# Kernel optimization log

Measured on AMD Instinct MI355X. Metric: run time of the kernel, lower is better.

Reference implementation:

```python
import jax, jax.numpy as jnp
import numpy as np

NEG_MIN = float(np.finfo(np.float32).min)
LN_EPS = 1e-05


def _layer_norm(x, g, b):
    m = jnp.mean(x, axis=-1, keepdims=True)
    v = jnp.var(x, axis=-1, keepdims=True)
    return (x - m) * jax.lax.rsqrt(v + LN_EPS) * g + b


def _rel_shift_uni(x):
    # x: [qlen, rlen, bsz, n_head] -- Transformer-XL relative shift
    q, r, b, n = x.shape
    zero_pad = jnp.zeros((q, 1, b, n), x.dtype)
    x_padded = jnp.concatenate([zero_pad, x], axis=1).reshape(r + 1, q, b, n)
    return x_padded[1:].reshape(q, r, b, n)


def setup_inputs() -> dict:
    key = jax.random.key(0)
    ks = jax.random.split(key, 12)
    qlen, bsz, d_model = 2048, 2, 1024
    n_head, d_head, d_inner = 16, 64, 4096

    w = jax.random.normal(ks[0], (qlen, bsz, d_model), dtype=jnp.float32)

    # sinusoidal relative position embedding, positions klen-1 .. 0
    pos_seq = jnp.arange(qlen - 1, -1, -1, dtype=jnp.float32)
    inv_freq = 1.0 / (10000.0 ** (jnp.arange(0, d_model, 2, dtype=jnp.float32) / d_model))
    sinusoid = pos_seq[:, None] * inv_freq[None, :]
    r = jnp.concatenate([jnp.sin(sinusoid), jnp.cos(sinusoid)], axis=-1)  # [qlen, d_model]

    s = 0.02
    r_w_bias = jax.random.normal(ks[1], (n_head, d_head), dtype=jnp.float32) * s
    r_r_bias = jax.random.normal(ks[2], (n_head, d_head), dtype=jnp.float32) * s
    qkv_w = jax.random.normal(ks[3], (d_model, 3 * n_head * d_head), dtype=jnp.float32) * s
    r_net_w = jax.random.normal(ks[4], (d_model, n_head * d_head), dtype=jnp.float32) * s
    o_w = jax.random.normal(ks[5], (n_head * d_head, d_model), dtype=jnp.float32) * s
    ffn_w1 = jax.random.normal(ks[6], (d_model, d_inner), dtype=jnp.float32) * s
    ffn_b1 = jnp.zeros((d_inner,), dtype=jnp.float32)
    ffn_w2 = jax.random.normal(ks[7], (d_inner, d_model), dtype=jnp.float32) * s
    ffn_b2 = jnp.zeros((d_model,), dtype=jnp.float32)
    ln1_g = jnp.ones((d_model,), dtype=jnp.float32)
    ln1_b = jnp.zeros((d_model,), dtype=jnp.float32)
    ln2_g = jnp.ones((d_model,), dtype=jnp.float32)
    ln2_b = jnp.zeros((d_model,), dtype=jnp.float32)

    # causal mask: position j > i is masked (uni-directional attention)
    attn_mask = jnp.triu(jnp.ones((qlen, qlen), dtype=bool), k=1)

    return {"w": w, "r": r, "r_w_bias": r_w_bias, "r_r_bias": r_r_bias,
            "attn_mask": attn_mask, "qkv_w": qkv_w, "r_net_w": r_net_w, "o_w": o_w,
            "ln1_g": ln1_g, "ln1_b": ln1_b, "ffn_w1": ffn_w1, "ffn_b1": ffn_b1,
            "ffn_w2": ffn_w2, "ffn_b2": ffn_b2, "ln2_g": ln2_g, "ln2_b": ln2_b}


def reference(w, r, r_w_bias, r_r_bias, attn_mask, qkv_w, r_net_w, o_w,
              ln1_g, ln1_b, ffn_w1, ffn_b1, ffn_w2, ffn_b2, ln2_g, ln2_b):
    qlen, bsz, d_model = w.shape
    n_head, d_head = r_w_bias.shape
    scale = 1.0 / (d_head ** 0.5)

    # qkv projection (post-lnorm path: no pre-norm)
    w_heads = w @ qkv_w  # [q, b, 3*n*d]
    w_q, w_k, w_v = jnp.split(w_heads, 3, axis=-1)
    w_q = w_q.reshape(qlen, bsz, n_head, d_head)
    w_k = w_k.reshape(qlen, bsz, n_head, d_head)
    w_v = w_v.reshape(qlen, bsz, n_head, d_head)

    r_k = (r @ r_net_w).reshape(r.shape[0], n_head, d_head)  # [rlen, n, d]

    # AC: content term, BD: position term with rel-shift
    AC = jnp.einsum('ibnd,jbnd->ijbn', w_q + r_w_bias, w_k)
    BD = jnp.einsum('ibnd,jnd->ijbn', w_q + r_r_bias, r_k)
    BD = _rel_shift_uni(BD)

    attn_score = (AC + BD) * scale
    attn_score = jnp.where(attn_mask[:, :, None, None], NEG_MIN, attn_score)
    attn_prob = jax.nn.softmax(attn_score, axis=1)  # softmax over key axis j

    attn_vec = jnp.einsum('ijbn,jbnd->ibnd', attn_prob, w_v)
    attn_vec = attn_vec.reshape(qlen, bsz, n_head * d_head)
    attn_out = attn_vec @ o_w

    x = _layer_norm(w + attn_out, ln1_g, ln1_b)  # post-lnorm

    # PositionwiseFF (post-lnorm, eval: dropout inactive)
    core = jax.nn.relu(x @ ffn_w1 + ffn_b1) @ ffn_w2 + ffn_b2
    out = _layer_norm(x + core, ln2_g, ln2_b)
    return out
```

## Files before the change

### kernel.cpp

```cpp
#include <hip/hip_runtime.h>
#include <math.h>


typedef __attribute__((ext_vector_type(8))) short short8;
typedef __attribute__((ext_vector_type(4))) float floatx4;

__device__ inline unsigned short f2bf(float f) {
  union { float f; unsigned u; } v; v.f = f;
  unsigned r = v.u + 0x7FFFu + ((v.u >> 16) & 1u);
  return (unsigned short)(r >> 16);
}
__device__ inline float bf2f(unsigned short u) {
  union { unsigned u; float f; } v; v.u = ((unsigned)u) << 16; return v.f;
}

__global__ __launch_bounds__(256) void prep_kernel(
    const float* __restrict__ w, unsigned short* __restrict__ wb,
    const float* __restrict__ r, unsigned short* __restrict__ rb,
    const float* __restrict__ qkv_w, unsigned short* __restrict__ qkvT,
    const float* __restrict__ r_net_w, unsigned short* __restrict__ rnetT,
    const float* __restrict__ o_w, unsigned short* __restrict__ owT,
    const float* __restrict__ ffn_w1, unsigned short* __restrict__ w1T,
    const float* __restrict__ ffn_w2, unsigned short* __restrict__ w2T) {
  __shared__ __align__(16) unsigned short Ts[64][68];
  const int blk = blockIdx.x;
  const int t = threadIdx.x;
  if (blk < 6144) {
    const float* in = blk < 4096 ? w : r;
    unsigned short* outp = blk < 4096 ? wb : rb;
    const int i = (blk < 4096 ? blk : blk - 4096) * 256 + t;
    float4 v = ((const float4*)in)[i];
    ((ushort4*)outp)[i] =
        make_ushort4(f2bf(v.x), f2bf(v.y), f2bf(v.z), f2bf(v.w));
    return;
  }
  const float* src; unsigned short* dst; int K, N, idx;
  if (blk < 6912)      { src = qkv_w;   dst = qkvT;  K = 1024; N = 3072; idx = blk - 6144; }
  else if (blk < 7168) { src = r_net_w; dst = rnetT; K = 1024; N = 1024; idx = blk - 6912; }
  else if (blk < 7424) { src = o_w;     dst = owT;   K = 1024; N = 1024; idx = blk - 7168; }
  else if (blk < 8448) { src = ffn_w1;  dst = w1T;   K = 1024; N = 4096; idx = blk - 7424; }
  else                 { src = ffn_w2;  dst = w2T;   K = 4096; N = 1024; idx = blk - 8448; }
  const int nbx = N >> 6;
  const int k0 = (idx / nbx) * 64, n0 = (idx % nbx) * 64;
  const int rr = t >> 4, c = (t & 15) * 4;
#pragma unroll
  for (int rb2 = 0; rb2 < 64; rb2 += 16) {
    float4 v = *(const float4*)(src + (size_t)(k0 + rb2 + rr) * N + n0 + c);
    *(ushort4*)&Ts[rb2 + rr][c] =
        make_ushort4(f2bf(v.x), f2bf(v.y), f2bf(v.z), f2bf(v.w));
  }
  __syncthreads();
#pragma unroll
  for (int rb2 = 0; rb2 < 64; rb2 += 16) {
    const int nn = rb2 + rr;
    ushort4 o = make_ushort4(Ts[c + 0][nn], Ts[c + 1][nn],
                             Ts[c + 2][nn], Ts[c + 3][nn]);
    *(ushort4*)(dst + (size_t)(n0 + nn) * K + k0 + c) = o;
  }
}

template<int BIAS, int RELU, int OUT_BF16>
__device__ __forceinline__ void bgemm_body(
    const unsigned short* __restrict__ A, const unsigned short* __restrict__ Bt,
    const float* __restrict__ bias, void* __restrict__ C,
    int M, int N, int Kstride, int Klen, size_t psize,
    int bx, int by, int kz,
    unsigned short* As, unsigned short* Bs) {
  const int t = threadIdx.x;
  const int wv = t >> 6, lane = t & 63, quad = lane >> 4, lq = lane & 15;
  const int m0 = by * 128, n0 = bx * 128;
  const int wvm = (wv >> 1) * 64, wvn = (wv & 1) * 64;

  const int srow = t >> 2;
  const int scol = (t & 3) * 8;
  const size_t koff = (size_t)kz * Klen;
  const unsigned short* Ag = A + (size_t)(m0 + srow) * Kstride + scol + koff;
  const unsigned short* Bg = Bt + (size_t)(n0 + srow) * Kstride + scol + koff;
  unsigned short* AsW0 = As + (size_t)wv * 512;
  unsigned short* AsW1 = As + 4096 + (size_t)wv * 512;
  unsigned short* BsW0 = Bs + (size_t)wv * 512;
  unsigned short* BsW1 = Bs + 4096 + (size_t)wv * 512;

  floatx4 acc[4][4];
#pragma unroll
  for (int am = 0; am < 4; ++am)
#pragma unroll
    for (int bn = 0; bn < 4; ++bn) acc[am][bn] = (floatx4){0.f, 0.f, 0.f, 0.f};

  for (int k0 = 0; k0 < Klen; k0 += 64) {
    __syncthreads();
    __builtin_amdgcn_global_load_lds(
        (const __attribute__((address_space(1))) void*)(Ag + k0),
        (__attribute__((address_space(3))) void*)AsW0, 16, 0, 0);
    __builtin_amdgcn_global_load_lds(
        (const __attribute__((address_space(1))) void*)(Ag + (size_t)64 * Kstride + k0),
        (__attribute__((address_space(3))) void*)(AsW0 + 64 * 32), 16, 0, 0);
    __builtin_amdgcn_global_load_lds(
        (const __attribute__((address_space(1))) void*)(Ag + k0 + 32),
        (__attribute__((address_space(3))) void*)AsW1, 16, 0, 0);
    __builtin_amdgcn_global_load_lds(
        (const __attribute__((address_space(1))) void*)(Ag + (size_t)64 * Kstride + k0 + 32),
        (__attribute__((address_space(3))) void*)(AsW1 + 64 * 32), 16, 0, 0);
    __builtin_amdgcn_global_load_lds(
        (const __attribute__((address_space(1))) void*)(Bg + k0),
        (__attribute__((address_space(3))) void*)BsW0, 16, 0, 0);
    __builtin_amdgcn_global_load_lds(
        (const __attribute__((address_space(1))) void*)(Bg + (size_t)64 * Kstride + k0),
        (__attribute__((address_space(3))) void*)(BsW0 + 64 * 32), 16, 0, 0);
    __builtin_amdgcn_global_load_lds(
        (const __attribute__((address_space(1))) void*)(Bg + k0 + 32),
        (__attribute__((address_space(3))) void*)BsW1, 16, 0, 0);
    __builtin_amdgcn_global_load_lds(
        (const __attribute__((address_space(1))) void*)(Bg + (size_t)64 * Kstride + k0 + 32),
        (__attribute__((address_space(3))) void*)(BsW1 + 64 * 32), 16, 0, 0);
    __syncthreads();

#pragma unroll
    for (int s = 0; s < 2; ++s) {
      const unsigned short* Asub = s ? As + 4096 : As;
      const unsigned short* Bsub = s ? Bs + 4096 : Bs;
      short8 af[4], bf[4];
#pragma unroll
      for (int am = 0; am < 4; ++am)
        af[am] = *(const short8*)&Asub[(wvm + am * 16 + lq) * 32 + quad * 8];
#pragma unroll
      for (int bn = 0; bn < 4; ++bn)
        bf[bn] = *(const short8*)&Bsub[(wvn + bn * 16 + lq) * 32 + quad * 8];
#pragma unroll
      for (int am = 0; am < 4; ++am)
#pragma unroll
        for (int bn = 0; bn < 4; ++bn)
          acc[am][bn] = __builtin_amdgcn_mfma_f32_16x16x32_bf16(
              af[am], bf[bn], acc[am][bn], 0, 0, 0);
    }
  }

  float bs[4] = {0.f, 0.f, 0.f, 0.f};
  if (BIAS) {
    if (kz == 0) {
#pragma unroll
      for (int bn = 0; bn < 4; ++bn) bs[bn] = bias[n0 + wvn + bn * 16 + lq];
    }
  }
  float* Cf = (float*)C + (size_t)kz * psize;
#pragma unroll
  for (int am = 0; am < 4; ++am) {
#pragma unroll
    for (int u = 0; u < 4; ++u) {
      const size_t row = m0 + wvm + am * 16 + quad * 4 + u;
#pragma unroll
      for (int bn = 0; bn < 4; ++bn) {
        const size_t col = n0 + wvn + bn * 16 + lq;
        float v = acc[am][bn][u];
        if (BIAS) v += bs[bn];
        if (RELU) v = fmaxf(v, 0.f);
        if (OUT_BF16) ((unsigned short*)C)[row * N + col] = f2bf(v);
        else          Cf[row * N + col] = v;
      }
    }
  }
}

template<int BIAS, int RELU, int OUT_BF16>
__global__ __launch_bounds__(256) void bgemm_kernel(
    const unsigned short* __restrict__ A, const unsigned short* __restrict__ Bt,
    const float* __restrict__ bias, void* __restrict__ C,
    int M, int N, int Kstride, int Klen, size_t psize) {
  __shared__ __align__(16) unsigned short As[2 * 128 * 32];
  __shared__ __align__(16) unsigned short Bs[2 * 128 * 32];
  bgemm_body<BIAS, RELU, OUT_BF16>(A, Bt, bias, C, M, N, Kstride, Klen, psize,
                                   blockIdx.x, blockIdx.y, blockIdx.z, As, Bs);
}

__global__ __launch_bounds__(256) void qkv_rk_kernel(
    const unsigned short* __restrict__ wb, const unsigned short* __restrict__ qkvT,
    unsigned short* __restrict__ w_heads,
    const unsigned short* __restrict__ rbf, const unsigned short* __restrict__ rnetT,
    unsigned short* __restrict__ rk) {
  __shared__ __align__(16) unsigned short As[2 * 128 * 32];
  __shared__ __align__(16) unsigned short Bs[2 * 128 * 32];
  const int bid = blockIdx.x;
  if (bid < 768) {
    bgemm_body<0, 0, 1>(wb, qkvT, nullptr, w_heads, 4096, 3072, 1024, 1024, 0,
                        bid % 24, bid / 24, 0, As, Bs);
  } else {
    const int b2 = bid - 768;
    bgemm_body<0, 0, 1>(rbf, rnetT, nullptr, rk, 2048, 1024, 1024, 1024, 0,
                        b2 % 8, b2 / 8, 0, As, Bs);
  }
}

__global__ __launch_bounds__(512, 4) void attn_mfma_kernel(
    const unsigned short* __restrict__ w_heads,
    const unsigned short* __restrict__ r_k,
    const float* __restrict__ r_w_bias, const float* __restrict__ r_r_bias,
    unsigned short* __restrict__ attn_vec) {
  __shared__ __align__(16) unsigned short Ks[64 * 72];
  __shared__ __align__(16) unsigned short Vt[64 * 72];
  __shared__ __align__(16) unsigned short Rb[256 * 72];
  __shared__ __align__(16) unsigned short Pl[8 * 16 * 72];

  const int t = threadIdx.x;
  const int wv = t >> 6, lane = t & 63, quad = lane >> 4, lq = lane & 15;
  const int g = blockIdx.x;
  const int qq = g >> 5, bnb = g & 31;
  const int it = (qq < 8) ? (15 - qq) : (qq - 8);
  const int b = bnb & 1, n = bnb >> 1;
  const int i0 = it * 128, iw = i0 + wv * 16;

  const int kr = t >> 3, kc8 = (t & 7) * 8;
  const int vj = t & 31, vc = (t >> 5) * 4;

  short8 qw[2], qr[2];
  {
    const unsigned short* qrow =
        w_heads + (size_t)((iw + lq) * 2 + b) * 3072 + n * 64;
    short8 a0 = *(const short8*)(qrow + quad * 8);
    short8 a1 = *(const short8*)(qrow + 32 + quad * 8);
    const float* wbp = r_w_bias + n * 64;
    const float* rbp = r_r_bias + n * 64;
#pragma unroll
    for (int j = 0; j < 8; ++j) {
      const int k0 = quad * 8 + j, k1 = 32 + quad * 8 + j;
      const float q0 = bf2f((unsigned short)a0[j]);
      const float q1 = bf2f((unsigned short)a1[j]);
      qw[0][j] = (short)f2bf(q0 + wbp[k0]);
      qr[0][j] = (short)f2bf(q0 + rbp[k0]);
      qw[1][j] = (short)f2bf(q1 + wbp[k1]);
      qr[1][j] = (short)f2bf(q1 + rbp[k1]);
    }
  }

  floatx4 o[4];
#pragma unroll
  for (int dt = 0; dt < 4; ++dt) o[dt] = (floatx4){0.f, 0.f, 0.f, 0.f};
  float lrow[4] = {0.f, 0.f, 0.f, 0.f};

  unsigned short* Pw = Pl + wv * (16 * 72);
  const int wb2 = 112 - wv * 16;

  int g_idx[4]; bool g_hi[4];
#pragma unroll
  for (int u = 0; u < 4; ++u) {
    const int s = 15 - (quad * 4 + u);
    g_idx[u] = quad * 16 + ((s + lq) & 15);
    g_hi[u] = (s + lq) >= 16;
  }

  const int pbase0 = 1920 - i0;
  const int jt_end = 2 * it + 2;

#pragma unroll
  for (int bq = 0; bq < 2; ++bq) {
    const int row = pbase0 + bq * 64 + kr;
    const int slot = row & 255;
    *(short8*)&Rb[slot * 72 + kc8] =
        *(const short8*)(r_k + (size_t)row * 1024 + n * 64 + kc8);
  }
  short8 sK, sR;
  ushort4 sVl, sVh;
  {
    const unsigned short* kb =
        w_heads + (size_t)(kr * 2 + b) * 3072 + n * 64 + 1024 + kc8;
    sK = *(const short8*)kb;
    const unsigned short* vbp =
        w_heads + (size_t)((2 * vj) * 2 + b) * 3072 + n * 64 + 2048 + vc;
    sVl = *(const ushort4*)vbp;
    sVh = *(const ushort4*)(vbp + 2 * 3072);
    int pg = pbase0 + 128 + kr; if (pg > 2047) pg = 2047;
    sR = *(const short8*)(r_k + (size_t)pg * 1024 + n * 64 + kc8);
  }

  for (int jt = 0; jt < jt_end; ++jt) {
    const int j0 = jt * 64;
    const int pbase = pbase0 + 64 * jt;

    asm volatile("" ::: "memory");
    __builtin_amdgcn_s_barrier();
    asm volatile("" ::: "memory");

    *(short8*)&Ks[kr * 72 + kc8] = sK;
#pragma unroll
    for (int i2 = 0; i2 < 4; ++i2)
      *(unsigned*)&Vt[(vc + i2) * 72 + 2 * vj] =
          (unsigned)sVl[i2] | ((unsigned)sVh[i2] << 16);
    {
      const int slot = (pbase + 128 + kr) & 255;
      *(short8*)&Rb[slot * 72 + kc8] = sR;
    }

    if (jt + 1 < jt_end) {
      const int j0n = j0 + 64;
      const unsigned short* kb =
          w_heads + (size_t)((j0n + kr) * 2 + b) * 3072 + n * 64 + 1024 + kc8;
      sK = *(const short8*)kb;
      const unsigned short* vbp =
          w_heads + (size_t)((j0n + 2 * vj) * 2 + b) * 3072 + n * 64 + 2048 + vc;
      sVl = *(const ushort4*)vbp;
      sVh = *(const ushort4*)(vbp + 2 * 3072);
      int pg = pbase + 192 + kr; if (pg > 2047) pg = 2047;
      sR = *(const short8*)(r_k + (size_t)pg * 1024 + n * 64 + kc8);
    }

    asm volatile("s_waitcnt lgkmcnt(0)" ::: "memory");
    __builtin_amdgcn_s_barrier();
    asm volatile("" ::: "memory");

    floatx4 ac[4];
#pragma unroll
    for (int ct = 0; ct < 4; ++ct) {
      short8 b0 = *(const short8*)&Ks[(ct * 16 + lq) * 72 + quad * 8];
      short8 b1 = *(const short8*)&Ks[(ct * 16 + lq) * 72 + 32 + quad * 8];
      floatx4 z = (floatx4){0.f, 0.f, 0.f, 0.f};
      z = __builtin_amdgcn_mfma_f32_16x16x32_bf16(qw[0], b0, z, 0, 0, 0);
      z = __builtin_amdgcn_mfma_f32_16x16x32_bf16(qw[1], b1, z, 0, 0, 0);
      ac[ct] = z;
    }
    floatx4 Tt[5];
#pragma unroll
    for (int pt = 0; pt < 5; ++pt) {
      const int slot = (pbase + wb2 + pt * 16 + lq) & 255;
      short8 b0 = *(const short8*)&Rb[slot * 72 + quad * 8];
      short8 b1 = *(const short8*)&Rb[slot * 72 + 32 + quad * 8];
      floatx4 z = (floatx4){0.f, 0.f, 0.f, 0.f};
      z = __builtin_amdgcn_mfma_f32_16x16x32_bf16(qr[0], b0, z, 0, 0, 0);
      z = __builtin_amdgcn_mfma_f32_16x16x32_bf16(qr[1], b1, z, 0, 0, 0);
      Tt[pt] = z;
    }

    const bool interior = (j0 + 63 <= iw);
    if (interior) {
#pragma unroll
      for (int u = 0; u < 4; ++u) {
        const int r = quad * 4 + u;
        float sh[5];
#pragma unroll
        for (int pt = 0; pt < 5; ++pt) sh[pt] = __shfl(Tt[pt][u], g_idx[u]);
#pragma unroll
        for (int ct = 0; ct < 4; ++ct) {
          const float bd = g_hi[u] ? sh[ct + 1] : sh[ct];
          const float xs = (ac[ct][u] + bd) * 0.18033688011112042f;
          float pr; asm("v_exp_f32 %0, %1" : "=v"(pr) : "v"(xs));
          Pw[r * 72 + ct * 16 + lq] = f2bf(pr);
          lrow[u] += pr;
        }
      }
    } else {
#pragma unroll
      for (int u = 0; u < 4; ++u) {
        const int r = quad * 4 + u, i = iw + r;
        float sh[5];
#pragma unroll
        for (int pt = 0; pt < 5; ++pt) sh[pt] = __shfl(Tt[pt][u], g_idx[u]);
#pragma unroll
        for (int ct = 0; ct < 4; ++ct) {
          const float bd = g_hi[u] ? sh[ct + 1] : sh[ct];
          const int j = j0 + ct * 16 + lq;
          const float xs = (ac[ct][u] + bd) * 0.18033688011112042f;
          float pr; asm("v_exp_f32 %0, %1" : "=v"(pr) : "v"(xs));
          pr = (j <= i) ? pr : 0.f;
          Pw[r * 72 + ct * 16 + lq] = f2bf(pr);
          lrow[u] += pr;
        }
      }
    }

    __builtin_amdgcn_s_waitcnt(0xC07F);

    short8 pA0 = *(const short8*)&Pw[lq * 72 + quad * 8];
    short8 pA1 = *(const short8*)&Pw[lq * 72 + 32 + quad * 8];
#pragma unroll
    for (int dt = 0; dt < 4; ++dt) {
      short8 v0 = *(const short8*)&Vt[(dt * 16 + lq) * 72 + quad * 8];
      short8 v1 = *(const short8*)&Vt[(dt * 16 + lq) * 72 + 32 + quad * 8];
      o[dt] = __builtin_amdgcn_mfma_f32_16x16x32_bf16(pA0, v0, o[dt], 0, 0, 0);
      o[dt] = __builtin_amdgcn_mfma_f32_16x16x32_bf16(pA1, v1, o[dt], 0, 0, 0);
    }
  }

#pragma unroll
  for (int u = 0; u < 4; ++u) {
    float l = lrow[u];
    l += __shfl_xor(l, 1);
    l += __shfl_xor(l, 2);
    l += __shfl_xor(l, 4);
    l += __shfl_xor(l, 8);
    const float linv = 1.f / l;
    const int i = iw + quad * 4 + u;
    unsigned short* op = attn_vec + (size_t)(i * 2 + b) * 1024 + n * 64 + lq;
#pragma unroll
    for (int dt = 0; dt < 4; ++dt) op[dt * 16] = f2bf(o[dt][u] * linv);
  }
}

__global__ __launch_bounds__(256) void ln_res_kernel(
    const float* __restrict__ X, const float* __restrict__ R0,
    const float* __restrict__ R1,
    const float* __restrict__ g, const float* __restrict__ bta,
    float* __restrict__ out, unsigned short* __restrict__ out_bf) {
  const int row = blockIdx.x;
  const int t = threadIdx.x;
  float4 xv = ((const float4*)(X + (size_t)row * 1024))[t];
  float4 rv = ((const float4*)(R0 + (size_t)row * 1024))[t];
  float4 v = make_float4(xv.x + rv.x, xv.y + rv.y, xv.z + rv.z, xv.w + rv.w);
  if (R1) {
    float4 r2 = ((const float4*)(R1 + (size_t)row * 1024))[t];
    v.x += r2.x; v.y += r2.y; v.z += r2.z; v.w += r2.w;
  }
  float s  = v.x + v.y + v.z + v.w;
  float sq = v.x * v.x + v.y * v.y + v.z * v.z + v.w * v.w;
#pragma unroll
  for (int off = 32; off > 0; off >>= 1) {
    s  += __shfl_xor(s, off);
    sq += __shfl_xor(sq, off);
  }
  __shared__ float ss[4], ssq[4];
  const int wid = t >> 6;
  if ((t & 63) == 0) { ss[wid] = s; ssq[wid] = sq; }
  __syncthreads();
  s  = ss[0] + ss[1] + ss[2] + ss[3];
  sq = ssq[0] + ssq[1] + ssq[2] + ssq[3];
  const float mean = s * (1.f / 1024.f);
  const float var  = sq * (1.f / 1024.f) - mean * mean;
  const float inv  = rsqrtf(var + 1e-5f);
  float4 gv = ((const float4*)g)[t];
  float4 bv = ((const float4*)bta)[t];
  float4 ov = make_float4((v.x - mean) * inv * gv.x + bv.x,
                          (v.y - mean) * inv * gv.y + bv.y,
                          (v.z - mean) * inv * gv.z + bv.z,
                          (v.w - mean) * inv * gv.w + bv.w);
  ((float4*)(out + (size_t)row * 1024))[t] = ov;
  if (out_bf)
    ((ushort4*)(out_bf + (size_t)row * 1024))[t] =
        make_ushort4(f2bf(ov.x), f2bf(ov.y), f2bf(ov.z), f2bf(ov.w));
}

extern "C" void kernel_launch(void* const* d_in, const int* in_sizes, int n_in,
                              void* d_out, int out_size, void* d_ws, size_t ws_size,
                              hipStream_t stream) {
  (void)in_sizes; (void)n_in; (void)out_size; (void)ws_size;
  const float* w        = (const float*)d_in[0];
  const float* r        = (const float*)d_in[1];
  const float* r_w_bias = (const float*)d_in[2];
  const float* r_r_bias = (const float*)d_in[3];
  const float* qkv_w    = (const float*)d_in[5];
  const float* r_net_w  = (const float*)d_in[6];
  const float* o_w      = (const float*)d_in[7];
  const float* ln1_g    = (const float*)d_in[8];
  const float* ln1_b    = (const float*)d_in[9];
  const float* ffn_w1   = (const float*)d_in[10];
  const float* ffn_b1   = (const float*)d_in[11];
  const float* ffn_w2   = (const float*)d_in[12];
  const float* ffn_b2   = (const float*)d_in[13];
  const float* ln2_g    = (const float*)d_in[14];
  const float* ln2_b    = (const float*)d_in[15];
  float* out = (float*)d_out;

  char* base = (char*)d_ws;
  const size_t MB = (size_t)1 << 20;
  unsigned short* w_heads = (unsigned short*)(base + 0);
  float*          aout0   = (float*)(base + 0);
  float*          aout1   = (float*)(base + 16 * MB);
  unsigned short* h1      = (unsigned short*)(base + 0);
  float*          x       = (float*)(base + 32 * MB);
  unsigned short* w2T     = (unsigned short*)(base + 48 * MB);
  unsigned short* w1T     = (unsigned short*)(base + 56 * MB);
  float*          core0   = (float*)(base + 56 * MB);
  float*          core1   = (float*)(base + 72 * MB);
  unsigned short* wb      = (unsigned short*)(base + 64 * MB);
  unsigned short* avec    = (unsigned short*)(base + 64 * MB);
  unsigned short* rb      = (unsigned short*)(base + 72 * MB);
  unsigned short* xb      = (unsigned short*)(base + 72 * MB);
  unsigned short* rk      = (unsigned short*)(base + 76 * MB);
  unsigned short* qkvT    = (unsigned short*)(base + 80 * MB);
  unsigned short* owT     = (unsigned short*)(base + 86 * MB);
  unsigned short* rnetT   = (unsigned short*)(base + 88 * MB);

  dim3 blk(256);
  prep_kernel<<<9472, blk, 0, stream>>>(w, wb, r, rb, qkv_w, qkvT,
                                        r_net_w, rnetT, o_w, owT,
                                        ffn_w1, w1T, ffn_w2, w2T);

  qkv_rk_kernel<<<896, blk, 0, stream>>>(wb, qkvT, w_heads, rb, rnetT, rk);
  attn_mfma_kernel<<<512, 512, 0, stream>>>(
      w_heads, rk, r_w_bias, r_r_bias, avec);
  bgemm_kernel<0, 0, 0><<<dim3(8, 32, 2), blk, 0, stream>>>(
      avec, owT, nullptr, aout0, 4096, 1024, 1024, 512, (size_t)4096 * 1024);
  ln_res_kernel<<<4096, blk, 0, stream>>>(w, aout0, aout1, ln1_g, ln1_b, x, xb);
  bgemm_kernel<1, 1, 1><<<dim3(32, 32, 1), blk, 0, stream>>>(
      xb, w1T, ffn_b1, h1, 4096, 4096, 1024, 1024, 0);
  bgemm_kernel<1, 0, 0><<<dim3(8, 32, 2), blk, 0, stream>>>(
      h1, w2T, ffn_b2, core0, 4096, 1024, 4096, 2048, (size_t)4096 * 1024);
  ln_res_kernel<<<4096, blk, 0, stream>>>(x, core0, core1, ln2_g, ln2_b, out, nullptr);
}
```

Before: 418.2 us.

## Add 256x256 double-buffered GEMM for QKV/r_k and FFN1 projections

Introduces a new GEMM body with 256x256 output tiles, 512 threads, K-step 64 and double-buffered LDS staging, so the next tile's global-to-LDS loads overlap MFMA compute. It replaces the 128x128 single-buffer GEMM for the fused QKV/r_k launch and the FFN first layer. Larger tiles cut global/L2 traffic per FLOP but use 128KB of LDS per block and many accumulator registers, which lowers occupancy and leaves fewer blocks (224 and 256) to fill the CUs. The LDS layout with 64-element rows and no padding may cause bank conflicts.

```diff
diff --git a/kernel.cpp b/kernel.cpp
--- a/kernel.cpp
+++ b/kernel.cpp
@@ -13,6 +13,11 @@
 __device__ inline float bf2f(unsigned short u) {
   union { unsigned u; float f; } v; v.u = ((unsigned)u) << 16; return v.f;
 }
+
+#define G2L(gp, lp)                                                  \
+  __builtin_amdgcn_global_load_lds(                                  \
+      (const __attribute__((address_space(1))) void*)(gp),           \
+      (__attribute__((address_space(3))) void*)(lp), 16, 0, 0)
 
 __global__ __launch_bounds__(256) void prep_kernel(
     const float* __restrict__ w, unsigned short* __restrict__ wb,
@@ -89,30 +94,14 @@
 
   for (int k0 = 0; k0 < Klen; k0 += 64) {
     __syncthreads();
-    __builtin_amdgcn_global_load_lds(
-        (const __attribute__((address_space(1))) void*)(Ag + k0),
-        (__attribute__((address_space(3))) void*)AsW0, 16, 0, 0);
-    __builtin_amdgcn_global_load_lds(
-        (const __attribute__((address_space(1))) void*)(Ag + (size_t)64 * Kstride + k0),
-        (__attribute__((address_space(3))) void*)(AsW0 + 64 * 32), 16, 0, 0);
-    __builtin_amdgcn_global_load_lds(
-        (const __attribute__((address_space(1))) void*)(Ag + k0 + 32),
-        (__attribute__((address_space(3))) void*)AsW1, 16, 0, 0);
-    __builtin_amdgcn_global_load_lds(
-        (const __attribute__((address_space(1))) void*)(Ag + (size_t)64 * Kstride + k0 + 32),
-        (__attribute__((address_space(3))) void*)(AsW1 + 64 * 32), 16, 0, 0);
-    __builtin_amdgcn_global_load_lds(
-        (const __attribute__((address_space(1))) void*)(Bg + k0),
-        (__attribute__((address_space(3))) void*)BsW0, 16, 0, 0);
-    __builtin_amdgcn_global_load_lds(
-        (const __attribute__((address_space(1))) void*)(Bg + (size_t)64 * Kstride + k0),
-        (__attribute__((address_space(3))) void*)(BsW0 + 64 * 32), 16, 0, 0);
-    __builtin_amdgcn_global_load_lds(
-        (const __attribute__((address_space(1))) void*)(Bg + k0 + 32),
-        (__attribute__((address_space(3))) void*)BsW1, 16, 0, 0);
-    __builtin_amdgcn_global_load_lds(
-        (const __attribute__((address_space(1))) void*)(Bg + (size_t)64 * Kstride + k0 + 32),
-        (__attribute__((address_space(3))) void*)(BsW1 + 64 * 32), 16, 0, 0);
+    G2L(Ag + k0, AsW0);
+    G2L(Ag + (size_t)64 * Kstride + k0, AsW0 + 64 * 32);
+    G2L(Ag + k0 + 32, AsW1);
+    G2L(Ag + (size_t)64 * Kstride + k0 + 32, AsW1 + 64 * 32);
+    G2L(Bg + k0, BsW0);
+    G2L(Bg + (size_t)64 * Kstride + k0, BsW0 + 64 * 32);
+    G2L(Bg + k0 + 32, BsW1);
+    G2L(Bg + (size_t)64 * Kstride + k0 + 32, BsW1 + 64 * 32);
     __syncthreads();
 
 #pragma unroll
@@ -172,21 +161,129 @@
                                    blockIdx.x, blockIdx.y, blockIdx.z, As, Bs);
 }
 
-__global__ __launch_bounds__(256) void qkv_rk_kernel(
+template<int BIAS, int RELU, int OUT_BF16>
+__device__ __forceinline__ void gemm256_body(
+    const unsigned short* __restrict__ A, const unsigned short* __restrict__ Bt,
+    const float* __restrict__ bias, void* __restrict__ C,
+    int N, int K, int bx, int by,
+    unsigned short* As0, unsigned short* As1,
+    unsigned short* Bs0, unsigned short* Bs1) {
+  const int t = threadIdx.x;
+  const int wv = t >> 6, lane = t & 63, quad = lane >> 4, lq = lane & 15;
+  const int wr = wv >> 2, wc = wv & 3;
+  const int m0 = by * 256, n0 = bx * 256;
+
+  const int srow = t >> 3, scol8 = (t & 7) * 8;
+  const unsigned short* Ag = A + (size_t)(m0 + srow) * K + scol8;
+  const unsigned short* Bg = Bt + (size_t)(n0 + srow) * K + scol8;
+
+  floatx4 acc[8][4];
+#pragma unroll
+  for (int am = 0; am < 8; ++am)
+#pragma unroll
+    for (int bn = 0; bn < 4; ++bn) acc[am][bn] = (floatx4){0.f, 0.f, 0.f, 0.f};
+
+#define STAGE256(Asb, Bsb, k0)                                         \
+  do {                                                                 \
+    _Pragma("unroll")                                                  \
+    for (int i = 0; i < 4; ++i) {                                      \
+      G2L(Ag + (size_t)(i * 64) * K + (k0), (Asb) + i * 4096 + wv * 512); \
+      G2L(Bg + (size_t)(i * 64) * K + (k0), (Bsb) + i * 4096 + wv * 512); \
+    }                                                                  \
+  } while (0)
+
+#define COMPUTE256(Asb, Bsb)                                           \
+  do {                                                                 \
+    _Pragma("unroll")                                                  \
+    for (int s = 0; s < 2; ++s) {                                      \
+      short8 af[8], bf[4];                                             \
+      _Pragma("unroll")                                                \
+      for (int am = 0; am < 8; ++am)                                   \
+        af[am] = *(const short8*)&(Asb)[(wr * 128 + am * 16 + lq) * 64 + \
+                                        s * 32 + quad * 8];            \
+      _Pragma("unroll")                                                \
+      for (int bn = 0; bn < 4; ++bn)                                   \
+        bf[bn] = *(const short8*)&(Bsb)[(wc * 64 + bn * 16 + lq) * 64 + \
+                                        s * 32 + quad * 8];            \
+      _Pragma("unroll")                                                \
+      for (int am = 0; am < 8; ++am)                                   \
+        _Pragma("unroll")                                              \
+        for (int bn = 0; bn < 4; ++bn)                                 \
+          acc[am][bn] = __builtin_amdgcn_mfma_f32_16x16x32_bf16(       \
+              af[am], bf[bn], acc[am][bn], 0, 0, 0);                   \
+    }                                                                  \
+  } while (0)
+
+  const int NT = K >> 6;
+  STAGE256(As0, Bs0, 0);
+  asm volatile("s_waitcnt vmcnt(0)" ::: "memory");
+  __builtin_amdgcn_s_barrier();
+
+  for (int kt = 0; kt + 1 < NT; ++kt) {
+    unsigned short* SA = (kt & 1) ? As0 : As1;
+    unsigned short* SB = (kt & 1) ? Bs0 : Bs1;
+    const unsigned short* CA = (kt & 1) ? As1 : As0;
+    const unsigned short* CB = (kt & 1) ? Bs1 : Bs0;
+    STAGE256(SA, SB, (kt + 1) * 64);
+    COMPUTE256(CA, CB);
+    asm volatile("s_waitcnt vmcnt(0)" ::: "memory");
+    __builtin_amdgcn_s_barrier();
+  }
+  if (NT & 1) COMPUTE256(As0, Bs0);
+  else        COMPUTE256(As1, Bs1);
+
+#undef STAGE256
+#undef COMPUTE256
+
+  float bs[4] = {0.f, 0.f, 0.f, 0.f};
+  if (BIAS) {
+#pragma unroll
+    for (int bn = 0; bn < 4; ++bn) bs[bn] = bias[n0 + wc * 64 + bn * 16 + lq];
+  }
+#pragma unroll
+  for (int am = 0; am < 8; ++am) {
+#pragma unroll
+    for (int u = 0; u < 4; ++u) {
+      const size_t row = m0 + wr * 128 + am * 16 + quad * 4 + u;
+#pragma unroll
+      for (int bn = 0; bn < 4; ++bn) {
+        const size_t col = n0 + wc * 64 + bn * 16 + lq;
+        float v = acc[am][bn][u];
+        if (BIAS) v += bs[bn];
+        if (RELU) v = fmaxf(v, 0.f);
+        if (OUT_BF16) ((unsigned short*)C)[row * N + col] = f2bf(v);
+        else          ((float*)C)[row * N + col] = v;
+      }
+    }
+  }
+}
+
+template<int BIAS, int RELU, int OUT_BF16>
+__global__ __launch_bounds__(512, 2) void gemm256_kernel(
+    const unsigned short* __restrict__ A, const unsigned short* __restrict__ Bt,
+    const float* __restrict__ bias, void* __restrict__ C, int N, int K) {
+  __shared__ __align__(16) unsigned short As[2][256 * 64];
+  __shared__ __align__(16) unsigned short Bs[2][256 * 64];
+  gemm256_body<BIAS, RELU, OUT_BF16>(A, Bt, bias, C, N, K,
+                                     blockIdx.x, blockIdx.y,
+                                     As[0], As[1], Bs[0], Bs[1]);
+}
+
+__global__ __launch_bounds__(512, 2) void qkv_rk256_kernel(
     const unsigned short* __restrict__ wb, const unsigned short* __restrict__ qkvT,
     unsigned short* __restrict__ w_heads,
     const unsigned short* __restrict__ rbf, const unsigned short* __restrict__ rnetT,
     unsigned short* __restrict__ rk) {
-  __shared__ __align__(16) unsigned short As[2 * 128 * 32];
-  __shared__ __align__(16) unsigned short Bs[2 * 128 * 32];
+  __shared__ __align__(16) unsigned short As[2][256 * 64];
+  __shared__ __align__(16) unsigned short Bs[2][256 * 64];
   const int bid = blockIdx.x;
-  if (bid < 768) {
-    bgemm_body<0, 0, 1>(wb, qkvT, nullptr, w_heads, 4096, 3072, 1024, 1024, 0,
-                        bid % 24, bid / 24, 0, As, Bs);
+  if (bid < 192) {
+    gemm256_body<0, 0, 1>(wb, qkvT, nullptr, w_heads, 3072, 1024,
+                          bid % 12, bid / 12, As[0], As[1], Bs[0], Bs[1]);
   } else {
-    const int b2 = bid - 768;
-    bgemm_body<0, 0, 1>(rbf, rnetT, nullptr, rk, 2048, 1024, 1024, 1024, 0,
-                        b2 % 8, b2 / 8, 0, As, Bs);
+    const int b2 = bid - 192;
+    gemm256_body<0, 0, 1>(rbf, rnetT, nullptr, rk, 1024, 1024,
+                          b2 % 4, b2 / 4, As[0], As[1], Bs[0], Bs[1]);
   }
 }
 
@@ -481,14 +578,14 @@
                                         r_net_w, rnetT, o_w, owT,
                                         ffn_w1, w1T, ffn_w2, w2T);
 
-  qkv_rk_kernel<<<896, blk, 0, stream>>>(wb, qkvT, w_heads, rb, rnetT, rk);
+  qkv_rk256_kernel<<<224, 512, 0, stream>>>(wb, qkvT, w_heads, rb, rnetT, rk);
   attn_mfma_kernel<<<512, 512, 0, stream>>>(
       w_heads, rk, r_w_bias, r_r_bias, avec);
   bgemm_kernel<0, 0, 0><<<dim3(8, 32, 2), blk, 0, stream>>>(
       avec, owT, nullptr, aout0, 4096, 1024, 1024, 512, (size_t)4096 * 1024);
   ln_res_kernel<<<4096, blk, 0, stream>>>(w, aout0, aout1, ln1_g, ln1_b, x, xb);
-  bgemm_kernel<1, 1, 1><<<dim3(32, 32, 1), blk, 0, stream>>>(
-      xb, w1T, ffn_b1, h1, 4096, 4096, 1024, 1024, 0);
+  gemm256_kernel<1, 1, 1><<<dim3(16, 16), 512, 0, stream>>>(
+      xb, w1T, ffn_b1, h1, 4096, 1024);
   bgemm_kernel<1, 0, 0><<<dim3(8, 32, 2), blk, 0, stream>>>(
       h1, w2T, ffn_b2, core0, 4096, 1024, 4096, 2048, (size_t)4096 * 1024);
   ln_res_kernel<<<4096, blk, 0, stream>>>(x, core0, core1, ln2_g, ln2_b, out, nullptr);
```

Measured after the change: 421.6 us. Within noise of the previous version (+0.8%).
